# Performance work log

Measured on AMD Instinct MI355X. Metric: run time of the kernel, lower is better.

## Reference

```python
import jax, jax.numpy as jnp
import numpy as np

H = 8   # num_heads
K = 7   # kernel_size


def setup_inputs() -> dict:
    key = jax.random.key(0)
    k1, k2, k3 = jax.random.split(key, 3)
    T, B, C = 2048, 16, 512
    x = jax.random.normal(k1, (T, B, C), dtype=jnp.float32)
    query = jax.random.normal(k2, (T, B, C), dtype=jnp.float32)
    W = jax.random.normal(k3, (C, H * K), dtype=jnp.float32) * 0.02
    return {"x": x, "query": query, "W": W}


def reference(x, query, W):
    T, B, C = x.shape
    R = C // H
    # per-position, per-head kernel weights: Dense(H*K) on query, no bias
    weight = jnp.einsum('tbc,cn->tbn', query, W).reshape(T * B * H, K)
    weight = jax.nn.softmax(weight, axis=-1)  # weight_softmax=True; dropout rate 0 is identity
    # TF extract_patches with SAME padding along T: total pad K-1, more on the bottom
    pad_before = (K - 1) // 2
    pad_after = K - 1 - pad_before
    x_pad = jnp.pad(x, ((pad_before, pad_after), (0, 0), (0, 0)))
    idx = jnp.arange(T)[:, None] + jnp.arange(K)[None, :]  # (T, K)
    patches = x_pad[idx]                      # (T, K, B, C)
    patches = jnp.transpose(patches, (0, 2, 1, 3))  # (T, B, K, C): TF depth order is (k, c)
    # Faithful to the source: flat (K*C) axis reinterpreted as (H, R, K)
    x_unfold = patches.reshape(T * B * H, R, K)
    out = jnp.einsum('nrk,nk->nr', x_unfold, weight)  # batched tiny matmul
    return out.reshape(T, B, C)
```

## Files before the change

kernel.cpp:

```cpp
#include <hip/hip_runtime.h>

#define T_DIM 2048
#define B_DIM 16
#define C_DIM 512
#define NW 56

#define XS_BYTES (22 * 512 * 2)
#define C_WT_OFF XS_BYTES
#define C_LDS    (XS_BYTES + 3584)

typedef __attribute__((ext_vector_type(8))) short short8;
typedef __attribute__((ext_vector_type(4))) float floatx4;

static __device__ __forceinline__ unsigned short f2bf(float x_) {
    union { float f; unsigned u; } v; v.f = x_;
    return (unsigned short)((v.u + 0x7FFFu + ((v.u >> 16) & 1u)) >> 16);
}
static __device__ __forceinline__ float bf_lo(unsigned u) {
    union { unsigned u; float f; } c; c.u = u << 16; return c.f;
}
static __device__ __forceinline__ float bf_hi(unsigned u) {
    union { unsigned u; float f; } c; c.u = u & 0xFFFF0000u; return c.f;
}
static __device__ __forceinline__ int swz(int a) { return a ^ ((a >> 3) & 0x70); }

__global__ __launch_bounds__(256)
void pack_w(const float* __restrict__ W, short8* __restrict__ Bg) {
    const int g  = blockIdx.x * 256 + threadIdx.x;
    const int ks = g >> 8;
    const int nt = (g >> 6) & 3;
    const int l  = g & 63;
    const int c  = l & 15;
    const int n  = nt * 14 + c;
    const int k0 = ks * 32 + ((l >> 4) & 3) * 8;
    short8 o;
#pragma unroll
    for (int j = 0; j < 8; ++j) {
        const float v = (c < 14) ? W[(size_t)(k0 + j) * NW + n] : 0.f;
        o[j] = (short)f2bf(v);
    }
    Bg[g] = o;
}

__global__ __launch_bounds__(256)
void weight2(const float* __restrict__ q, const short8* __restrict__ Bg,
             float* __restrict__ wt_g) {
    __shared__ __align__(16) short8 A8[16 * 64];

    const int tid  = threadIdx.x;
    const int lane = tid & 63;
    const int wv   = tid >> 6;
    const int b    = blockIdx.x & 15;
    const int t0   = (blockIdx.x >> 4) * 16;

    const int rq = lane & 15;
    const int qq = lane >> 4;
    const float* qrow = q + ((size_t)(t0 + rq) * B_DIM + b) * C_DIM + qq * 8;
#pragma unroll
    for (int s = 0; s < 4; ++s) {
        const int ks = wv + s * 4;
        const float4 f0 = *(const float4*)(qrow + ks * 32);
        const float4 f1 = *(const float4*)(qrow + ks * 32 + 4);
        short8 o;
        o[0] = (short)f2bf(f0.x); o[1] = (short)f2bf(f0.y);
        o[2] = (short)f2bf(f0.z); o[3] = (short)f2bf(f0.w);
        o[4] = (short)f2bf(f1.x); o[5] = (short)f2bf(f1.y);
        o[6] = (short)f2bf(f1.z); o[7] = (short)f2bf(f1.w);
        A8[ks * 64 + lane] = o;
    }
    __syncthreads();

    floatx4 acc = (floatx4){0.f, 0.f, 0.f, 0.f};
#pragma unroll
    for (int ks = 0; ks < 16; ++ks) {
        const short8 bf = Bg[(ks * 4 + wv) * 64 + lane];
        acc = __builtin_amdgcn_mfma_f32_16x16x32_bf16(A8[ks * 64 + lane], bf,
                                                      acc, 0, 0, 0);
    }

    const int c    = lane & 15;
    const int cb   = (c < 7) ? 0 : 7;
    const int sb   = (lane & 48) + cb;
    const int quad = lane >> 4;
#pragma unroll
    for (int r = 0; r < 4; ++r) {
        const float a = acc[r];
        const float v0 = __shfl(a, sb + 0);
        const float v1 = __shfl(a, sb + 1);
        const float v2 = __shfl(a, sb + 2);
        const float v3 = __shfl(a, sb + 3);
        const float v4 = __shfl(a, sb + 4);
        const float v5 = __shfl(a, sb + 5);
        const float v6 = __shfl(a, sb + 6);
        const float mx = fmaxf(fmaxf(fmaxf(v0, v1), fmaxf(v2, v3)),
                               fmaxf(fmaxf(v4, v5), v6));
        const float sm = __expf(v0 - mx) + __expf(v1 - mx) + __expf(v2 - mx) +
                         __expf(v3 - mx) + __expf(v4 - mx) + __expf(v5 - mx) +
                         __expf(v6 - mx);
        const float w = __expf(a - mx) * (1.0f / sm);
        if (c < 14)
            wt_g[((size_t)(t0 + quad * 4 + r) * B_DIM + b) * NW + wv * 14 + c] = w;
    }
}

__global__ __launch_bounds__(512)
void conv2(const float* __restrict__ x, const float* __restrict__ wt_g,
           float* __restrict__ out) {
    __shared__ __align__(16) char S[C_LDS];

    const int tid  = threadIdx.x;
    const int lane = tid & 63;
    const int wv   = tid >> 6;
    const int b    = blockIdx.x & 15;
    const int t0   = (blockIdx.x >> 4) * 16;

    float4 xr[6];
#pragma unroll
    for (int j = 0; j < 6; ++j) {
        const int idx = tid + j * 512;
        xr[j] = make_float4(0.f, 0.f, 0.f, 0.f);
        if (idx < 2816) {
            const int i  = idx >> 7;
            const int cc = (idx & 127) * 4;
            const int tp = t0 + i - 3;
            if (tp >= 0 && tp < T_DIM)
                xr[j] = *(const float4*)(x + ((size_t)tp * B_DIM + b) * C_DIM + cc);
        }
    }
    float4 wld = make_float4(0.f, 0.f, 0.f, 0.f);
    const int wrow = tid / 14;
    const int wj   = tid - wrow * 14;
    if (tid < 224)
        wld = *(const float4*)(wt_g + ((size_t)(t0 + wrow) * B_DIM + b) * NW + wj * 4);

    char* XS = S;
#pragma unroll
    for (int j = 0; j < 6; ++j) {
        const int idx = tid + j * 512;
        if (idx < 2816) {
            uint2 p;
            p.x = (unsigned)f2bf(xr[j].x) | ((unsigned)f2bf(xr[j].y) << 16);
            p.y = (unsigned)f2bf(xr[j].z) | ((unsigned)f2bf(xr[j].w) << 16);
            *(uint2*)(XS + swz(idx * 8)) = p;
        }
    }
    if (tid < 224)
        *(float4*)(S + C_WT_OFF + (wrow * NW + wj * 4) * 4) = wld;
    __syncthreads();

    const float* wt = (const float*)(S + C_WT_OFF);
    const int h = lane >> 3;
    const int base_b = lane * 112;
#pragma unroll
    for (int s = 0; s < 2; ++s) {
        const int tt = wv * 2 + s;
        const int tb = tt * 1024 + base_b;
        uint4 xu[7];
#pragma unroll
        for (int i = 0; i < 7; ++i)
            xu[i] = *(const uint4*)(XS + swz(tb + i * 16));
        float xf[56];
#pragma unroll
        for (int i = 0; i < 7; ++i) {
            xf[i * 8 + 0] = bf_lo(xu[i].x); xf[i * 8 + 1] = bf_hi(xu[i].x);
            xf[i * 8 + 2] = bf_lo(xu[i].y); xf[i * 8 + 3] = bf_hi(xu[i].y);
            xf[i * 8 + 4] = bf_lo(xu[i].z); xf[i * 8 + 5] = bf_hi(xu[i].z);
            xf[i * 8 + 6] = bf_lo(xu[i].w); xf[i * 8 + 7] = bf_hi(xu[i].w);
        }
        const float* wp = wt + tt * NW + h * 7;
        float w[7];
#pragma unroll
        for (int k = 0; k < 7; ++k) w[k] = wp[k];
        float a8[8];
#pragma unroll
        for (int r = 0; r < 8; ++r) {
            float sacc = xf[r * 7] * w[0];
#pragma unroll
            for (int k = 1; k < 7; ++k) sacc = fmaf(w[k], xf[r * 7 + k], sacc);
            a8[r] = sacc;
        }
        float* orow = out + ((size_t)(t0 + tt) * B_DIM + b) * C_DIM + lane * 8;
        const floatx4 v0 = (floatx4){a8[0], a8[1], a8[2], a8[3]};
        const floatx4 v1 = (floatx4){a8[4], a8[5], a8[6], a8[7]};
        __builtin_nontemporal_store(v0, (floatx4*)orow);
        __builtin_nontemporal_store(v1, (floatx4*)(orow + 4));
    }
}

extern "C" void kernel_launch(void* const* d_in, const int* in_sizes, int n_in,
                              void* d_out, int out_size, void* d_ws, size_t ws_size,
                              hipStream_t stream) {
    const float* x = (const float*)d_in[0];
    const float* q = (const float*)d_in[1];
    const float* W = (const float*)d_in[2];
    float* out = (float*)d_out;
    short8* Bg  = (short8*)d_ws;
    float* wt_g = (float*)((char*)d_ws + 65536);

    pack_w<<<16, 256, 0, stream>>>(W, Bg);
    weight2<<<(T_DIM / 16) * B_DIM, 256, 0, stream>>>(q, Bg, wt_g);
    conv2<<<(T_DIM / 16) * B_DIM, 512, 0, stream>>>(x, wt_g, out);
}
```

Measured before the change: 183.8 us.

## Fuse weight projection+softmax into conv kernel, keeping weights in LDS

Merges the query-projection/softmax kernel into the convolution kernel. Each block now loads its query tile and x tile together, runs the MFMA projection and softmax on four waves, and writes the softmax weights to LDS instead of global memory. This removes one kernel launch and the global write and re-read of the weight tensor, and lets the query and x loads overlap. In exchange it uses more LDS per block, adds a second barrier with half the waves idle during the projection, and switches the output stores from nontemporal to normal stores.

```diff
diff --git a/kernel.cpp b/kernel.cpp
--- a/kernel.cpp
+++ b/kernel.cpp
@@ -5,9 +5,11 @@
 #define C_DIM 512
 #define NW 56
 
+#define A_BYTES  16384
+#define XS_OFF   A_BYTES
 #define XS_BYTES (22 * 512 * 2)
-#define C_WT_OFF XS_BYTES
-#define C_LDS    (XS_BYTES + 3584)
+#define WT_OFF   (A_BYTES + XS_BYTES)
+#define F_LDS    (WT_OFF + 16 * NW * 4)
 
 typedef __attribute__((ext_vector_type(8))) short short8;
 typedef __attribute__((ext_vector_type(4))) float floatx4;
@@ -23,6 +25,9 @@
     union { unsigned u; float f; } c; c.u = u & 0xFFFF0000u; return c.f;
 }
 static __device__ __forceinline__ int swz(int a) { return a ^ ((a >> 3) & 0x70); }
+static __device__ __forceinline__ int aswz(int a) {
+    return a ^ ((((a >> 8) ^ (a >> 11)) & 7) << 4);
+}
 
 __global__ __launch_bounds__(256)
 void pack_w(const float* __restrict__ W, short8* __restrict__ Bg) {
@@ -42,10 +47,10 @@
     Bg[g] = o;
 }
 
-__global__ __launch_bounds__(256)
-void weight2(const float* __restrict__ q, const short8* __restrict__ Bg,
-             float* __restrict__ wt_g) {
-    __shared__ __align__(16) short8 A8[16 * 64];
+__global__ __launch_bounds__(512, 6)
+void fused3(const float* __restrict__ x, const float* __restrict__ q,
+            const short8* __restrict__ Bg, float* __restrict__ out) {
+    __shared__ __align__(16) char S[F_LDS];
 
     const int tid  = threadIdx.x;
     const int lane = tid & 63;
@@ -53,67 +58,14 @@
     const int b    = blockIdx.x & 15;
     const int t0   = (blockIdx.x >> 4) * 16;
 
-    const int rq = lane & 15;
-    const int qq = lane >> 4;
-    const float* qrow = q + ((size_t)(t0 + rq) * B_DIM + b) * C_DIM + qq * 8;
+    float4 qr[4];
 #pragma unroll
-    for (int s = 0; s < 4; ++s) {
-        const int ks = wv + s * 4;
-        const float4 f0 = *(const float4*)(qrow + ks * 32);
-        const float4 f1 = *(const float4*)(qrow + ks * 32 + 4);
-        short8 o;
-        o[0] = (short)f2bf(f0.x); o[1] = (short)f2bf(f0.y);
-        o[2] = (short)f2bf(f0.z); o[3] = (short)f2bf(f0.w);
-        o[4] = (short)f2bf(f1.x); o[5] = (short)f2bf(f1.y);
-        o[6] = (short)f2bf(f1.z); o[7] = (short)f2bf(f1.w);
-        A8[ks * 64 + lane] = o;
+    for (int j = 0; j < 4; ++j) {
+        const int idx = tid + j * 512;
+        const int r   = idx >> 7;
+        const int cc  = (idx & 127) * 4;
+        qr[j] = *(const float4*)(q + ((size_t)(t0 + r) * B_DIM + b) * C_DIM + cc);
     }
-    __syncthreads();
-
-    floatx4 acc = (floatx4){0.f, 0.f, 0.f, 0.f};
-#pragma unroll
-    for (int ks = 0; ks < 16; ++ks) {
-        const short8 bf = Bg[(ks * 4 + wv) * 64 + lane];
-        acc = __builtin_amdgcn_mfma_f32_16x16x32_bf16(A8[ks * 64 + lane], bf,
-                                                      acc, 0, 0, 0);
-    }
-
-    const int c    = lane & 15;
-    const int cb   = (c < 7) ? 0 : 7;
-    const int sb   = (lane & 48) + cb;
-    const int quad = lane >> 4;
-#pragma unroll
-    for (int r = 0; r < 4; ++r) {
-        const float a = acc[r];
-        const float v0 = __shfl(a, sb + 0);
-        const float v1 = __shfl(a, sb + 1);
-        const float v2 = __shfl(a, sb + 2);
-        const float v3 = __shfl(a, sb + 3);
-        const float v4 = __shfl(a, sb + 4);
-        const float v5 = __shfl(a, sb + 5);
-        const float v6 = __shfl(a, sb + 6);
-        const float mx = fmaxf(fmaxf(fmaxf(v0, v1), fmaxf(v2, v3)),
-                               fmaxf(fmaxf(v4, v5), v6));
-        const float sm = __expf(v0 - mx) + __expf(v1 - mx) + __expf(v2 - mx) +
-                         __expf(v3 - mx) + __expf(v4 - mx) + __expf(v5 - mx) +
-                         __expf(v6 - mx);
-        const float w = __expf(a - mx) * (1.0f / sm);
-        if (c < 14)
-            wt_g[((size_t)(t0 + quad * 4 + r) * B_DIM + b) * NW + wv * 14 + c] = w;
-    }
-}
-
-__global__ __launch_bounds__(512)
-void conv2(const float* __restrict__ x, const float* __restrict__ wt_g,
-           float* __restrict__ out) {
-    __shared__ __align__(16) char S[C_LDS];
-
-    const int tid  = threadIdx.x;
-    const int lane = tid & 63;
-    const int wv   = tid >> 6;
-    const int b    = blockIdx.x & 15;
-    const int t0   = (blockIdx.x >> 4) * 16;
-
     float4 xr[6];
 #pragma unroll
     for (int j = 0; j < 6; ++j) {
@@ -127,13 +79,21 @@
                 xr[j] = *(const float4*)(x + ((size_t)tp * B_DIM + b) * C_DIM + cc);
         }
     }
-    float4 wld = make_float4(0.f, 0.f, 0.f, 0.f);
-    const int wrow = tid / 14;
-    const int wj   = tid - wrow * 14;
-    if (tid < 224)
-        wld = *(const float4*)(wt_g + ((size_t)(t0 + wrow) * B_DIM + b) * NW + wj * 4);
 
-    char* XS = S;
+    char* AS = S;
+#pragma unroll
+    for (int j = 0; j < 4; ++j) {
+        const int idx = tid + j * 512;
+        const int r   = idx >> 7;
+        const int cc  = (idx & 127) * 4;
+        const int a   = (cc >> 5) * 1024 + ((cc >> 3) & 3) * 256 + r * 16 +
+                        (cc & 7) * 2;
+        uint2 p;
+        p.x = (unsigned)f2bf(qr[j].x) | ((unsigned)f2bf(qr[j].y) << 16);
+        p.y = (unsigned)f2bf(qr[j].z) | ((unsigned)f2bf(qr[j].w) << 16);
+        *(uint2*)(AS + aswz(a)) = p;
+    }
+    char* XS = S + XS_OFF;
 #pragma unroll
     for (int j = 0; j < 6; ++j) {
         const int idx = tid + j * 512;
@@ -144,11 +104,43 @@
             *(uint2*)(XS + swz(idx * 8)) = p;
         }
     }
-    if (tid < 224)
-        *(float4*)(S + C_WT_OFF + (wrow * NW + wj * 4) * 4) = wld;
     __syncthreads();
 
-    const float* wt = (const float*)(S + C_WT_OFF);
+    float* wt = (float*)(S + WT_OFF);
+    if (wv < 4) {
+        floatx4 acc = (floatx4){0.f, 0.f, 0.f, 0.f};
+#pragma unroll
+        for (int ks = 0; ks < 16; ++ks) {
+            const short8 af = *(const short8*)(AS + aswz(ks * 1024 + lane * 16));
+            const short8 bf = Bg[(ks * 4 + wv) * 64 + lane];
+            acc = __builtin_amdgcn_mfma_f32_16x16x32_bf16(af, bf, acc, 0, 0, 0);
+        }
+        const int c    = lane & 15;
+        const int cb   = (c < 7) ? 0 : 7;
+        const int sb   = (lane & 48) + cb;
+        const int quad = lane >> 4;
+#pragma unroll
+        for (int r = 0; r < 4; ++r) {
+            const float a = acc[r];
+            const float v0 = __shfl(a, sb + 0);
+            const float v1 = __shfl(a, sb + 1);
+            const float v2 = __shfl(a, sb + 2);
+            const float v3 = __shfl(a, sb + 3);
+            const float v4 = __shfl(a, sb + 4);
+            const float v5 = __shfl(a, sb + 5);
+            const float v6 = __shfl(a, sb + 6);
+            const float mx = fmaxf(fmaxf(fmaxf(v0, v1), fmaxf(v2, v3)),
+                                   fmaxf(fmaxf(v4, v5), v6));
+            const float sm = __expf(v0 - mx) + __expf(v1 - mx) + __expf(v2 - mx) +
+                             __expf(v3 - mx) + __expf(v4 - mx) + __expf(v5 - mx) +
+                             __expf(v6 - mx);
+            const float w = __expf(a - mx) * (1.0f / sm);
+            if (c < 14)
+                wt[(quad * 4 + r) * NW + wv * 14 + c] = w;
+        }
+    }
+    __syncthreads();
+
     const int h = lane >> 3;
     const int base_b = lane * 112;
 #pragma unroll
@@ -180,10 +172,8 @@
             a8[r] = sacc;
         }
         float* orow = out + ((size_t)(t0 + tt) * B_DIM + b) * C_DIM + lane * 8;
-        const floatx4 v0 = (floatx4){a8[0], a8[1], a8[2], a8[3]};
-        const floatx4 v1 = (floatx4){a8[4], a8[5], a8[6], a8[7]};
-        __builtin_nontemporal_store(v0, (floatx4*)orow);
-        __builtin_nontemporal_store(v1, (floatx4*)(orow + 4));
+        *(float4*)(orow)     = make_float4(a8[0], a8[1], a8[2], a8[3]);
+        *(float4*)(orow + 4) = make_float4(a8[4], a8[5], a8[6], a8[7]);
     }
 }
 
@@ -194,10 +184,8 @@
     const float* q = (const float*)d_in[1];
     const float* W = (const float*)d_in[2];
     float* out = (float*)d_out;
-    short8* Bg  = (short8*)d_ws;
-    float* wt_g = (float*)((char*)d_ws + 65536);
+    short8* Bg = (short8*)d_ws;
 
     pack_w<<<16, 256, 0, stream>>>(W, Bg);
-    weight2<<<(T_DIM / 16) * B_DIM, 256, 0, stream>>>(q, Bg, wt_g);
-    conv2<<<(T_DIM / 16) * B_DIM, 512, 0, stream>>>(x, wt_g, out);
+    fused3<<<(T_DIM / 16) * B_DIM, 512, 0, stream>>>(x, q, Bg, out);
 }
```

Result: faster. 176.0 us (-4.2%).
